# Kernel tuning notes

Measured on AMD Instinct MI355X. Metric: run time of the kernel, lower is better.

Reference implementation:

```python
import jax, jax.numpy as jnp
import numpy as np

N_NODES = 100000
N_EDGES = 1600000
IN_CH = 64
HID = 64


def setup_inputs() -> dict:
    key = jax.random.key(0)
    ks = jax.random.split(key, 7)
    x = jax.random.normal(ks[0], (N_NODES, IN_CH), dtype=jnp.float32)
    edge_index = jax.random.randint(ks[1], (2, N_EDGES), 0, N_NODES, dtype=jnp.int64)
    node_pair = jax.random.randint(ks[2], (2,), 0, N_NODES, dtype=jnp.int64)
    W1 = jax.random.normal(ks[3], (IN_CH, HID), dtype=jnp.float32) / np.float32(np.sqrt(IN_CH))
    b1 = jnp.zeros((HID,), dtype=jnp.float32)
    W2 = jax.random.normal(ks[4], (HID, HID), dtype=jnp.float32) / np.float32(np.sqrt(HID))
    b2 = jnp.zeros((HID,), dtype=jnp.float32)
    fc_W = jax.random.normal(ks[5], (2 * HID, 1), dtype=jnp.float32) / np.float32(np.sqrt(2 * HID))
    fc_b = jnp.zeros((1,), dtype=jnp.float32)
    return {"x": x, "edge_index": edge_index, "node_pair": node_pair,
            "W1": W1, "b1": b1, "W2": W2, "b2": b2, "fc_W": fc_W, "fc_b": fc_b}


def gcn_conv(x, W, b, src, dst, n):
    # linear transform then symmetric-normalized scatter-add with self-loops (PyG GCNConv)
    h = x @ W                                   # [n, out]
    loop = jnp.arange(n, dtype=src.dtype)
    s = jnp.concatenate([src, loop])            # [E+n]
    d = jnp.concatenate([dst, loop])
    deg = jax.ops.segment_sum(jnp.ones_like(d, dtype=h.dtype), d, num_segments=n)
    dinv = jnp.where(deg > 0, jax.lax.rsqrt(deg), 0.0)
    norm = dinv[s] * dinv[d]                    # [E+n]
    out = jax.ops.segment_sum(h[s] * norm[:, None], d, num_segments=n)
    return out + b


def reference(x, edge_index, node_pair, W1, b1, W2, b2, fc_W, fc_b):
    src, dst = edge_index[0], edge_index[1]
    n = x.shape[0]
    h = jax.nn.relu(gcn_conv(x, W1, b1, src, dst, n))
    h = jax.nn.relu(gcn_conv(h, W2, b2, src, dst, n))
    z = jnp.concatenate([h[node_pair[0]], h[node_pair[1]]], axis=0)  # [2*HID]
    return jax.nn.sigmoid(z @ fc_W + fc_b)      # [1]
```

## Files before the change

### kernel.cpp

```cpp
#include <hip/hip_runtime.h>
#include <math.h>


#define CH 64
#define E1CAP 4096
#define F1CAP (E1CAP + 2)
#define E2CAP 131072
#define SCAN_GRID 512
#define KD_GRID 128
#define TPB 256

struct Params {
    const float* x; const int* src; const int* dst; int E; int N;
    const int* np_;
    const float* W1; const float* b1; const float* W2; const float* b2;
    const float* fcW; const float* fcb;
    float* out;
    int* ctrl;
    int* deg; unsigned* bmF1; unsigned* bmNd;
    float* agg1e; int* pos1; int* e1s; int* e1d; int* F1;
    int* e2s; int* e2d; float* h1;
};

__device__ __forceinline__ float dinv_of(int degv) { return rsqrtf((float)(degv + 1)); }

__device__ __forceinline__ void ast(int* p_, int v) {
    __hip_atomic_store(p_, v, __ATOMIC_RELAXED, __HIP_MEMORY_SCOPE_AGENT);
}
__device__ __forceinline__ int ald(const int* p_) {
    return __hip_atomic_load(p_, __ATOMIC_RELAXED, __HIP_MEMORY_SCOPE_AGENT);
}
__device__ __forceinline__ float aldf(const float* p_) {
    return __hip_atomic_load(p_, __ATOMIC_RELAXED, __HIP_MEMORY_SCOPE_AGENT);
}

__device__ __forceinline__ bool last_arrive(int* cnt, int nblk) {
    __shared__ int is_last;
    __syncthreads();
    if (threadIdx.x == 0) {
        int t = __hip_atomic_fetch_add(cnt, 1, __ATOMIC_RELAXED, __HIP_MEMORY_SCOPE_AGENT);
        is_last = (t == nblk - 1) ? 1 : 0;
    }
    __syncthreads();
    return is_last != 0;
}

__global__ __launch_bounds__(TPB) void kA(Params p) {
    const int tid = blockIdx.x * blockDim.x + threadIdx.x;
    const int nthreads = gridDim.x * blockDim.x;
    const int p0 = p.np_[0], p1 = p.np_[1];
    const int nvec = p.E >> 2;
    const int4* dst4 = (const int4*)p.dst;

    for (int i = tid; i < nvec; i += nthreads) {
        int4 d4 = dst4[i];
        int ds[4] = {d4.x, d4.y, d4.z, d4.w};
#pragma unroll
        for (int k = 0; k < 4; k++) {
            int d = ds[k];
            if (d == p0 || d == p1) {
                int s = p.src[i * 4 + k];
                int idx = atomicAdd(&p.ctrl[0], 1);
                if (idx < E1CAP) { ast(&p.e1s[idx], s); ast(&p.e1d[idx], d); }
            }
        }
    }
    for (int e = (nvec << 2) + tid; e < p.E; e += nthreads) {
        int d = p.dst[e];
        if (d == p0 || d == p1) {
            int s = p.src[e];
            int idx = atomicAdd(&p.ctrl[0], 1);
            if (idx < E1CAP) { ast(&p.e1s[idx], s); ast(&p.e1d[idx], d); }
        }
    }

    if (!last_arrive(&p.ctrl[8], SCAN_GRID)) return;

    int cnt1 = min(ald(&p.ctrl[0]), E1CAP);
    for (int g = threadIdx.x; g < cnt1 + 2; g += TPB) {
        int u = (g < cnt1) ? ald(&p.e1s[g]) : ((g - cnt1) ? p1 : p0);
        unsigned bit = 1u << (u & 31);
        unsigned old = atomicOr(&p.bmF1[u >> 5], bit);
        if (!(old & bit)) {
            atomicOr(&p.bmNd[u >> 5], bit);
            int i = atomicAdd(&p.ctrl[2], 1);
            p.F1[i] = u;
            p.pos1[u] = i;
        }
    }
    __syncthreads();
    int nf1 = min(ald(&p.ctrl[2]), F1CAP);
    float4 z4 = make_float4(0.f, 0.f, 0.f, 0.f);
    float4* a4 = (float4*)p.agg1e;
    for (int i = threadIdx.x; i < nf1 * (CH / 4); i += TPB) a4[i] = z4;
}

__global__ __launch_bounds__(TPB) void kB(Params p) {
    const int tid = blockIdx.x * blockDim.x + threadIdx.x;
    const int nthreads = gridDim.x * blockDim.x;
    const int nvec = p.E >> 2;
    const int4* dst4 = (const int4*)p.dst;
    for (int i = tid; i < nvec; i += nthreads) {
        int4 d4 = dst4[i];
        int ds[4] = {d4.x, d4.y, d4.z, d4.w};
#pragma unroll
        for (int k = 0; k < 4; k++) {
            int d = ds[k];
            if ((p.bmF1[d >> 5] >> (d & 31)) & 1u) {
                int s = p.src[i * 4 + k];
                atomicOr(&p.bmNd[s >> 5], 1u << (s & 31));
                int idx = atomicAdd(&p.ctrl[1], 1);
                if (idx < E2CAP) { p.e2s[idx] = s; p.e2d[idx] = d; }
            }
        }
    }
    for (int e = (nvec << 2) + tid; e < p.E; e += nthreads) {
        int d = p.dst[e];
        if ((p.bmF1[d >> 5] >> (d & 31)) & 1u) {
            int s = p.src[e];
            atomicOr(&p.bmNd[s >> 5], 1u << (s & 31));
            int idx = atomicAdd(&p.ctrl[1], 1);
            if (idx < E2CAP) { p.e2s[idx] = s; p.e2d[idx] = d; }
        }
    }
}

__global__ __launch_bounds__(TPB) void kC(Params p) {
    const int tid = blockIdx.x * blockDim.x + threadIdx.x;
    const int nthreads = gridDim.x * blockDim.x;
    const int nvec = p.E >> 2;
    const int4* dst4 = (const int4*)p.dst;
    for (int i = tid; i < nvec; i += nthreads) {
        int4 d4 = dst4[i];
        int ds[4] = {d4.x, d4.y, d4.z, d4.w};
#pragma unroll
        for (int k = 0; k < 4; k++) {
            int d = ds[k];
            if ((p.bmNd[d >> 5] >> (d & 31)) & 1u) atomicAdd(&p.deg[d], 1);
        }
    }
    for (int e = (nvec << 2) + tid; e < p.E; e += nthreads) {
        int d = p.dst[e];
        if ((p.bmNd[d >> 5] >> (d & 31)) & 1u) atomicAdd(&p.deg[d], 1);
    }
}

__global__ __launch_bounds__(TPB) void kD(Params p) {
    const int tid = blockIdx.x * blockDim.x + threadIdx.x;
    const int nthreads = gridDim.x * blockDim.x;

    {
        int cnt2 = min(p.ctrl[1], E2CAP);
        long total = (long)cnt2 * CH;
        for (long idx = tid; idx < total; idx += nthreads) {
            int e = (int)(idx >> 6);
            int c = (int)(idx & 63);
            int w = p.e2s[e], u = p.e2d[e];
            float nrm = dinv_of(p.deg[w]) * dinv_of(p.deg[u]);
            atomicAdd(&p.agg1e[p.pos1[u] * CH + c], nrm * p.x[(size_t)w * CH + c]);
        }
    }

    if (!last_arrive(&p.ctrl[9], KD_GRID)) return;

    const int p0 = p.np_[0], p1 = p.np_[1];
    int nf1 = min(p.ctrl[2], F1CAP);
    int wave = threadIdx.x >> 6, lane = threadIdx.x & 63;
    for (int i = wave; i < nf1; i += TPB / 64) {
        int u = p.F1[i];
        float di = dinv_of(p.deg[u]);
        float aval = aldf(&p.agg1e[i * CH + lane]) + di * di * p.x[(size_t)u * CH + lane];
        float sum = p.b1[lane];
#pragma unroll 8
        for (int k = 0; k < CH; k++)
            sum += __shfl(aval, k) * p.W1[k * CH + lane];
        p.h1[i * CH + lane] = fmaxf(sum, 0.f);
    }
    __syncthreads();

    __shared__ float a[2][CH];
    __shared__ float partial[2];
    int t = threadIdx.x >> 6, j = threadIdx.x & 63;
    if (threadIdx.x < 128) {
        int pp = t ? p1 : p0;
        float dp = dinv_of(p.deg[pp]);
        float acc = dp * dp * p.h1[p.pos1[pp] * CH + j];
        int cnt1 = min(p.ctrl[0], E1CAP);
        for (int e = 0; e < cnt1; e++) {
            if (p.e1d[e] == pp) {
                int s = p.e1s[e];
                acc += dinv_of(p.deg[s]) * dp * p.h1[p.pos1[s] * CH + j];
            }
        }
        a[t][j] = acc;
    }
    __syncthreads();
    if (threadIdx.x < 128) {
        float sum = p.b2[j];
#pragma unroll
        for (int k = 0; k < CH; k++) sum += a[t][k] * p.W2[k * CH + j];
        float v = fmaxf(sum, 0.f);
        float pr = v * p.fcW[t * CH + j];
        for (int off = 32; off > 0; off >>= 1) pr += __shfl_down(pr, off);
        if (j == 0) partial[t] = pr;
    }
    __syncthreads();
    if (threadIdx.x == 0) {
        float z = partial[0] + partial[1] + p.fcb[0];
        p.out[0] = 1.f / (1.f + expf(-z));
    }
}

extern "C" void kernel_launch(void* const* d_in, const int* in_sizes, int n_in,
                              void* d_out, int out_size, void* d_ws, size_t ws_size,
                              hipStream_t stream) {
    Params p;
    p.x   = (const float*)d_in[0];
    const int* ei = (const int*)d_in[1];
    p.np_ = (const int*)d_in[2];
    p.W1  = (const float*)d_in[3];
    p.b1  = (const float*)d_in[4];
    p.W2  = (const float*)d_in[5];
    p.b2  = (const float*)d_in[6];
    p.fcW = (const float*)d_in[7];
    p.fcb = (const float*)d_in[8];
    p.out = (float*)d_out;

    p.N = in_sizes[0] / CH;
    p.E = in_sizes[1] / 2;
    p.src = ei;
    p.dst = ei + p.E;

    char* w = (char*)d_ws;
    size_t off = 0;
    auto alloc = [&](size_t bytes) {
        size_t o = off;
        off = (off + bytes + 255) & ~((size_t)255);
        return o;
    };
    size_t o_ctrl  = alloc(256);
    int bmN = (p.N + 31) / 32;
    size_t o_bmF1  = alloc((size_t)bmN * 4);
    size_t o_bmNd  = alloc((size_t)bmN * 4);
    size_t o_deg   = alloc((size_t)p.N * 4);
    size_t zero_end = off;
    size_t o_agg1e = alloc((size_t)F1CAP * CH * 4);
    size_t o_pos   = alloc((size_t)p.N * 4);
    size_t o_e1s   = alloc((size_t)E1CAP * 4);
    size_t o_e1d   = alloc((size_t)E1CAP * 4);
    size_t o_F1    = alloc((size_t)F1CAP * 4);
    size_t o_e2s   = alloc((size_t)E2CAP * 4);
    size_t o_e2d   = alloc((size_t)E2CAP * 4);
    size_t o_h1    = alloc((size_t)F1CAP * CH * 4);
    (void)ws_size;

    p.ctrl  = (int*)(w + o_ctrl);
    p.bmF1  = (unsigned*)(w + o_bmF1);
    p.bmNd  = (unsigned*)(w + o_bmNd);
    p.deg   = (int*)(w + o_deg);
    p.agg1e = (float*)(w + o_agg1e);
    p.pos1  = (int*)(w + o_pos);
    p.e1s   = (int*)(w + o_e1s);
    p.e1d   = (int*)(w + o_e1d);
    p.F1    = (int*)(w + o_F1);
    p.e2s   = (int*)(w + o_e2s);
    p.e2d   = (int*)(w + o_e2d);
    p.h1    = (float*)(w + o_h1);

    hipMemsetAsync(d_ws, 0, zero_end, stream);
    kA<<<SCAN_GRID, TPB, 0, stream>>>(p);
    kB<<<SCAN_GRID, TPB, 0, stream>>>(p);
    kC<<<SCAN_GRID, TPB, 0, stream>>>(p);
    kD<<<KD_GRID, TPB, 0, stream>>>(p);
}
```

Measured before the change: 149.6 us.

## Split fused last-block kernels into separate launches and enlarge scan grids

Replaces the last-arriving-block pattern in the scan and scatter kernels with separate single-block kernels (build frontier, tail compute), dropping the atomic loads, stores and arrival counters. The scan kernels now use one thread per int4 of edges (up to 8192 blocks) instead of a fixed 512-block grid, and the scatter uses 256 blocks. This trades two extra kernel launches for more parallelism in the memory-bound edge scans and no inter-block arrival synchronisation.

```diff
diff --git a/kernel.cpp b/kernel.cpp
--- a/kernel.cpp
+++ b/kernel.cpp
@@ -6,8 +6,6 @@
 #define E1CAP 4096
 #define F1CAP (E1CAP + 2)
 #define E2CAP 131072
-#define SCAN_GRID 512
-#define KD_GRID 128
 #define TPB 256
 
 struct Params {
@@ -24,34 +22,12 @@
 
 __device__ __forceinline__ float dinv_of(int degv) { return rsqrtf((float)(degv + 1)); }
 
-__device__ __forceinline__ void ast(int* p_, int v) {
-    __hip_atomic_store(p_, v, __ATOMIC_RELAXED, __HIP_MEMORY_SCOPE_AGENT);
-}
-__device__ __forceinline__ int ald(const int* p_) {
-    return __hip_atomic_load(p_, __ATOMIC_RELAXED, __HIP_MEMORY_SCOPE_AGENT);
-}
-__device__ __forceinline__ float aldf(const float* p_) {
-    return __hip_atomic_load(p_, __ATOMIC_RELAXED, __HIP_MEMORY_SCOPE_AGENT);
-}
-
-__device__ __forceinline__ bool last_arrive(int* cnt, int nblk) {
-    __shared__ int is_last;
-    __syncthreads();
-    if (threadIdx.x == 0) {
-        int t = __hip_atomic_fetch_add(cnt, 1, __ATOMIC_RELAXED, __HIP_MEMORY_SCOPE_AGENT);
-        is_last = (t == nblk - 1) ? 1 : 0;
-    }
-    __syncthreads();
-    return is_last != 0;
-}
-
-__global__ __launch_bounds__(TPB) void kA(Params p) {
+__global__ __launch_bounds__(TPB) void k1_e1(Params p) {
     const int tid = blockIdx.x * blockDim.x + threadIdx.x;
     const int nthreads = gridDim.x * blockDim.x;
     const int p0 = p.np_[0], p1 = p.np_[1];
     const int nvec = p.E >> 2;
     const int4* dst4 = (const int4*)p.dst;
-
     for (int i = tid; i < nvec; i += nthreads) {
         int4 d4 = dst4[i];
         int ds[4] = {d4.x, d4.y, d4.z, d4.w};
@@ -61,7 +37,7 @@
             if (d == p0 || d == p1) {
                 int s = p.src[i * 4 + k];
                 int idx = atomicAdd(&p.ctrl[0], 1);
-                if (idx < E1CAP) { ast(&p.e1s[idx], s); ast(&p.e1d[idx], d); }
+                if (idx < E1CAP) { p.e1s[idx] = s; p.e1d[idx] = d; }
             }
         }
     }
@@ -70,15 +46,16 @@
         if (d == p0 || d == p1) {
             int s = p.src[e];
             int idx = atomicAdd(&p.ctrl[0], 1);
-            if (idx < E1CAP) { ast(&p.e1s[idx], s); ast(&p.e1d[idx], d); }
-        }
-    }
-
-    if (!last_arrive(&p.ctrl[8], SCAN_GRID)) return;
-
-    int cnt1 = min(ald(&p.ctrl[0]), E1CAP);
+            if (idx < E1CAP) { p.e1s[idx] = s; p.e1d[idx] = d; }
+        }
+    }
+}
+
+__global__ __launch_bounds__(TPB) void k2_build(Params p) {
+    int cnt1 = min(p.ctrl[0], E1CAP);
+    const int p0 = p.np_[0], p1 = p.np_[1];
     for (int g = threadIdx.x; g < cnt1 + 2; g += TPB) {
-        int u = (g < cnt1) ? ald(&p.e1s[g]) : ((g - cnt1) ? p1 : p0);
+        int u = (g < cnt1) ? p.e1s[g] : ((g - cnt1) ? p1 : p0);
         unsigned bit = 1u << (u & 31);
         unsigned old = atomicOr(&p.bmF1[u >> 5], bit);
         if (!(old & bit)) {
@@ -89,13 +66,13 @@
         }
     }
     __syncthreads();
-    int nf1 = min(ald(&p.ctrl[2]), F1CAP);
+    int nf1 = min(p.ctrl[2], F1CAP);
     float4 z4 = make_float4(0.f, 0.f, 0.f, 0.f);
     float4* a4 = (float4*)p.agg1e;
     for (int i = threadIdx.x; i < nf1 * (CH / 4); i += TPB) a4[i] = z4;
 }
 
-__global__ __launch_bounds__(TPB) void kB(Params p) {
+__global__ __launch_bounds__(TPB) void k3_e2(Params p) {
     const int tid = blockIdx.x * blockDim.x + threadIdx.x;
     const int nthreads = gridDim.x * blockDim.x;
     const int nvec = p.E >> 2;
@@ -125,7 +102,7 @@
     }
 }
 
-__global__ __launch_bounds__(TPB) void kC(Params p) {
+__global__ __launch_bounds__(TPB) void k4_deg(Params p) {
     const int tid = blockIdx.x * blockDim.x + threadIdx.x;
     const int nthreads = gridDim.x * blockDim.x;
     const int nvec = p.E >> 2;
@@ -145,31 +122,29 @@
     }
 }
 
-__global__ __launch_bounds__(TPB) void kD(Params p) {
-    const int tid = blockIdx.x * blockDim.x + threadIdx.x;
-    const int nthreads = gridDim.x * blockDim.x;
-
-    {
-        int cnt2 = min(p.ctrl[1], E2CAP);
-        long total = (long)cnt2 * CH;
-        for (long idx = tid; idx < total; idx += nthreads) {
-            int e = (int)(idx >> 6);
-            int c = (int)(idx & 63);
-            int w = p.e2s[e], u = p.e2d[e];
-            float nrm = dinv_of(p.deg[w]) * dinv_of(p.deg[u]);
-            atomicAdd(&p.agg1e[p.pos1[u] * CH + c], nrm * p.x[(size_t)w * CH + c]);
-        }
-    }
-
-    if (!last_arrive(&p.ctrl[9], KD_GRID)) return;
-
+__global__ __launch_bounds__(TPB) void k5_scatter(Params p) {
+    const int tid = blockIdx.x * blockDim.x + threadIdx.x;
+    const int nthreads = gridDim.x * blockDim.x;
+    int cnt2 = min(p.ctrl[1], E2CAP);
+    long total = (long)cnt2 * CH;
+    for (long idx = tid; idx < total; idx += nthreads) {
+        int e = (int)(idx >> 6);
+        int c = (int)(idx & 63);
+        int w = p.e2s[e], u = p.e2d[e];
+        float nrm = dinv_of(p.deg[w]) * dinv_of(p.deg[u]);
+        atomicAdd(&p.agg1e[p.pos1[u] * CH + c], nrm * p.x[(size_t)w * CH + c]);
+    }
+}
+
+__global__ __launch_bounds__(TPB) void k6_tail(Params p) {
     const int p0 = p.np_[0], p1 = p.np_[1];
     int nf1 = min(p.ctrl[2], F1CAP);
     int wave = threadIdx.x >> 6, lane = threadIdx.x & 63;
+
     for (int i = wave; i < nf1; i += TPB / 64) {
         int u = p.F1[i];
         float di = dinv_of(p.deg[u]);
-        float aval = aldf(&p.agg1e[i * CH + lane]) + di * di * p.x[(size_t)u * CH + lane];
+        float aval = p.agg1e[i * CH + lane] + di * di * p.x[(size_t)u * CH + lane];
         float sum = p.b1[lane];
 #pragma unroll 8
         for (int k = 0; k < CH; k++)
@@ -268,8 +243,15 @@
     p.h1    = (float*)(w + o_h1);
 
     hipMemsetAsync(d_ws, 0, zero_end, stream);
-    kA<<<SCAN_GRID, TPB, 0, stream>>>(p);
-    kB<<<SCAN_GRID, TPB, 0, stream>>>(p);
-    kC<<<SCAN_GRID, TPB, 0, stream>>>(p);
-    kD<<<KD_GRID, TPB, 0, stream>>>(p);
-}
+
+    int scanBlocks = (p.E / 4 + TPB - 1) / TPB;
+    if (scanBlocks < 1) scanBlocks = 1;
+    if (scanBlocks > 8192) scanBlocks = 8192;
+
+    k1_e1     <<<scanBlocks, TPB, 0, stream>>>(p);
+    k2_build  <<<1,          TPB, 0, stream>>>(p);
+    k3_e2     <<<scanBlocks, TPB, 0, stream>>>(p);
+    k4_deg    <<<scanBlocks, TPB, 0, stream>>>(p);
+    k5_scatter<<<256,        TPB, 0, stream>>>(p);
+    k6_tail   <<<1,          TPB, 0, stream>>>(p);
+}
```

Measured after the change: 134.2 us. -10.3%, faster.
